# Optimization experiments

Hardware: AMD Instinct MI355X
Metric: run time of the kernel (lower is better)

The kernel has to match this reference:

```python
import jax, jax.numpy as jnp
import numpy as np

N = 100000   # nodes
E = 3200000  # edges
F = 128      # input features
H1 = 128     # first_gcn_dimensions
H2 = 64      # second_gcn_dimensions
D1 = 64      # first_dense_neurons
D2 = 8       # second_dense_neurons
L = 10       # number_of_labels


def setup_inputs() -> dict:
    key = jax.random.key(0)
    ks = jax.random.split(key, 8)
    edges = jax.random.randint(ks[0], (2, E), 0, N)
    features = jax.random.normal(ks[1], (N, F), dtype=jnp.float32)
    s = lambda k, shape: jax.random.normal(k, shape, dtype=jnp.float32) * 0.05
    return dict(
        edges=edges, features=features,
        W1=s(ks[2], (F, H1)), b1=jnp.zeros((H1,), jnp.float32),
        W2=s(ks[3], (H1, H2)), b2=jnp.zeros((H2,), jnp.float32),
        Wf1=s(ks[4], (H2, D1)), bf1=jnp.zeros((D1,), jnp.float32),
        Wf2=s(ks[5], (D1, D2)), bf2=jnp.zeros((D2,), jnp.float32),
        Wl=s(ks[6], (H2 * D2, L)), bl=jnp.zeros((L,), jnp.float32),
    )


def gcn_conv(x, W, b, src, dst, n):
    # PyG GCNConv: x' = D^{-1/2} (A + I) D^{-1/2} (x W) + b  (self-loops already in src/dst)
    h = x @ W                                            # [N, out]
    deg = jax.ops.segment_sum(jnp.ones(dst.shape[0], x.dtype), dst, num_segments=n)
    dinv = jnp.where(deg > 0, jax.lax.rsqrt(deg), 0.0)   # deg^{-1/2}, 0 for isolated
    norm = dinv[src] * dinv[dst]                         # [E+N]
    agg = jax.ops.segment_sum(h[src] * norm[:, None], dst, num_segments=n)
    return agg + b


def reference(edges, features, W1, b1, W2, b2, Wf1, bf1, Wf2, bf2, Wl, bl):
    n = features.shape[0]
    loop = jnp.arange(n)
    src = jnp.concatenate([edges[0], loop])
    dst = jnp.concatenate([edges[1], loop])

    h1 = jax.nn.relu(gcn_conv(features, W1, b1, src, dst, n))  # [N, H1]
    h2 = gcn_conv(h1, W2, b2, src, dst, n)                     # [N, H2]

    a1 = jnp.tanh(h2 @ Wf1 + bf1)                              # [N, D1]
    att = jax.nn.softmax(a1 @ Wf2 + bf2, axis=0)               # softmax over nodes, [N, D2]

    graph_embedding = (att.T @ h2).reshape(1, -1)              # [1, D2*H2]
    P = att.T @ att - jnp.eye(att.shape[1], dtype=att.dtype)   # [D2, D2]
    penalty = jnp.sum(jnp.sqrt(jnp.sum(P * P, axis=1)))

    predictions = jax.nn.log_softmax(graph_embedding @ Wl + bl, axis=1)  # [1, L]
    return graph_embedding, penalty, predictions
```

## Files before the change

kernel.cpp:

```cpp
#include <hip/hip_runtime.h>
#include <hip/hip_bf16.h>
#include <math.h>

#define NNODES 100000
#define NEDGES 3200000
#define NBUK ((NNODES + 127) >> 7)
#define NCHUNK 256
#define EPC (NEDGES / NCHUNK)

typedef float floatx2 __attribute__((ext_vector_type(2)));

__device__ __forceinline__ unsigned short f2bf(float x) {
    unsigned u = __float_as_uint(x);
    unsigned r = u + 0x7FFFu + ((u >> 16) & 1u);
    return (unsigned short)(r >> 16);
}
__device__ __forceinline__ void unpack8_bf16(uint4 v, float* f) {
    f[0] = __uint_as_float(v.x << 16); f[1] = __uint_as_float(v.x & 0xFFFF0000u);
    f[2] = __uint_as_float(v.y << 16); f[3] = __uint_as_float(v.y & 0xFFFF0000u);
    f[4] = __uint_as_float(v.z << 16); f[5] = __uint_as_float(v.z & 0xFFFF0000u);
    f[6] = __uint_as_float(v.w << 16); f[7] = __uint_as_float(v.w & 0xFFFF0000u);
}

__device__ __forceinline__ void acc8_fp8(uint2 v, floatx2* a) {
    a[0] += __builtin_amdgcn_cvt_pk_f32_fp8(v.x, false);
    a[1] += __builtin_amdgcn_cvt_pk_f32_fp8(v.x, true);
    a[2] += __builtin_amdgcn_cvt_pk_f32_fp8(v.y, false);
    a[3] += __builtin_amdgcn_cvt_pk_f32_fp8(v.y, true);
}
__device__ __forceinline__ void acc4_fp8(unsigned v, floatx2* a) {
    a[0] += __builtin_amdgcn_cvt_pk_f32_fp8(v, false);
    a[1] += __builtin_amdgcn_cvt_pk_f32_fp8(v, true);
}

__global__ __launch_bounds__(1024) void chunk_hist_kernel(const int* __restrict__ dst,
                                                          int* __restrict__ hist) {
    __shared__ int h[NBUK];
    int c = blockIdx.x, t = threadIdx.x;
    for (int i = t; i < NBUK; i += 1024) h[i] = 0;
    __syncthreads();
    int e0 = c * EPC, e1 = e0 + EPC;
    for (int e = e0 + t; e < e1; e += 1024)
        atomicAdd(&h[dst[e] >> 7], 1);
    __syncthreads();
    for (int i = t; i < NBUK; i += 1024)
        hist[c * NBUK + i] = h[i];
}

__global__ void col_scan_kernel(int* __restrict__ hist, int* __restrict__ btot) {
    int t = blockIdx.x * 256 + threadIdx.x;
    if (t >= NBUK) return;
    int run = 0;
    for (int c = 0; c < NCHUNK; c++) {
        int idx = c * NBUK + t;
        int v = hist[idx];
        hist[idx] = run;
        run += v;
    }
    btot[t] = run;
}

__global__ void bucket_scan_kernel(const int* __restrict__ btot, int* __restrict__ bstart,
                                   int* __restrict__ row_start, float* __restrict__ smalls) {
    __shared__ int s[1024];
    int t = threadIdx.x;
    if (t < 592) smalls[t] = 0.0f;
    int v = (t < NBUK) ? btot[t] : 0;
    s[t] = v;
    __syncthreads();
    for (int off = 1; off < 1024; off <<= 1) {
        int x = (t >= off) ? s[t - off] : 0;
        __syncthreads();
        s[t] += x;
        __syncthreads();
    }
    if (t < NBUK) bstart[t] = s[t] - v;
    if (t == 0) {
        bstart[NBUK] = NEDGES;
        row_start[NNODES] = NEDGES;
    }
}

__global__ __launch_bounds__(1024) void chunk_scatter_kernel(const int* __restrict__ src,
                                                             const int* __restrict__ dst,
                                                             const int* __restrict__ hist,
                                                             const int* __restrict__ bstart,
                                                             int* __restrict__ ebuk) {
    __shared__ int cur[NBUK];
    int c = blockIdx.x, t = threadIdx.x;
    for (int i = t; i < NBUK; i += 1024)
        cur[i] = bstart[i] + hist[c * NBUK + i];
    __syncthreads();
    int e0 = c * EPC, e1 = e0 + EPC;
    for (int e = e0 + t; e < e1; e += 1024) {
        int d = dst[e];
        int pos = atomicAdd(&cur[d >> 7], 1);
        ebuk[pos] = src[e] | ((d & 127) << 20);
    }
}

__global__ __launch_bounds__(256) void build_kernel(const int* __restrict__ ebuk,
                                                    const int* __restrict__ bstart,
                                                    int* __restrict__ row_start,
                                                    float* __restrict__ dinv,
                                                    int* __restrict__ csr) {
    __shared__ int cnt[128];
    __shared__ int scn[128];
    __shared__ int cur[128];
    int b = blockIdx.x;
    int t = threadIdx.x;
    int s0 = bstart[b], s1 = bstart[b + 1];
    if (t < 128) cnt[t] = 0;
    __syncthreads();
    for (int i = s0 + t; i < s1; i += 256)
        atomicAdd(&cnt[(ebuk[i] >> 20) & 127], 1);
    __syncthreads();
    if (t < 128) scn[t] = cnt[t];
    __syncthreads();
#pragma unroll
    for (int off = 1; off < 128; off <<= 1) {
        int x = (t < 128 && t >= off) ? scn[t - off] : 0;
        __syncthreads();
        if (t < 128) scn[t] += x;
        __syncthreads();
    }
    int node = b * 128 + t;
    if (t < 128) {
        int rs = s0 + scn[t] - cnt[t];
        cur[t] = rs;
        if (node < NNODES) {
            row_start[node] = rs;
            dinv[node] = rsqrtf((float)cnt[t] + 1.0f);
        }
    }
    __syncthreads();
    for (int i = s0 + t; i < s1; i += 256) {
        int v = ebuk[i];
        int pos = atomicAdd(&cur[(v >> 20) & 127], 1);
        csr[pos] = v & 0xFFFFF;
    }
}

template <int KIN, int KOUT, int TR>
__global__ __launch_bounds__(256) void gemm_stage_kernel(const float* __restrict__ A,
                                                         const float* __restrict__ W,
                                                         const float* __restrict__ rowscale,
                                                         unsigned char* __restrict__ stage,
                                                         int nrows) {
    constexpr int COLG = KOUT / 4;
    constexpr int ROWG = 256 / COLG;
    constexpr int R    = TR / ROWG;
    constexpr int LDK  = KIN + 4;
    __shared__ float As[TR][LDK];
    int block_row = blockIdx.x * TR;
    int tid = threadIdx.x;

    constexpr int C4 = KIN / 4;
    for (int idx = tid; idx < TR * C4; idx += 256) {
        int r = idx / C4, c = idx % C4;
        float4 v = make_float4(0.f, 0.f, 0.f, 0.f);
        if (block_row + r < nrows)
            v = *(const float4*)(A + (size_t)(block_row + r) * KIN + c * 4);
        *(float4*)(&As[r][c * 4]) = v;
    }
    __syncthreads();

    int cg = tid % COLG, rg = tid / COLG;
    int j  = cg * 4;
    int r0 = rg * R;
    float4 acc[R];
#pragma unroll
    for (int r = 0; r < R; r++) acc[r] = make_float4(0.f, 0.f, 0.f, 0.f);

#pragma unroll 4
    for (int k = 0; k < KIN; k++) {
        float4 w = *(const float4*)(W + (size_t)k * KOUT + j);
#pragma unroll
        for (int r = 0; r < R; r++) {
            float a = As[r0 + r][k];
            acc[r].x += a * w.x; acc[r].y += a * w.y;
            acc[r].z += a * w.z; acc[r].w += a * w.w;
        }
    }
#pragma unroll
    for (int r = 0; r < R; r++) {
        int row = block_row + r0 + r;
        if (row < nrows) {
            float d = rowscale[row];
            int pk = __builtin_amdgcn_cvt_pk_fp8_f32(acc[r].x * d, acc[r].y * d, 0, false);
            pk = __builtin_amdgcn_cvt_pk_fp8_f32(acc[r].z * d, acc[r].w * d, pk, true);
            *(unsigned*)(stage + (size_t)row * KOUT + j) = (unsigned)pk;
        }
    }
}

template <int KIN, int KOUT, int TR>
__global__ __launch_bounds__(256) void gemm_stage_bf16_kernel(const unsigned short* __restrict__ A,
                                                              const float* __restrict__ W,
                                                              const float* __restrict__ rowscale,
                                                              unsigned char* __restrict__ stage,
                                                              int nrows) {
    constexpr int COLG = KOUT / 4;
    constexpr int ROWG = 256 / COLG;
    constexpr int R    = TR / ROWG;
    constexpr int LDK  = KIN + 4;
    __shared__ float As[TR][LDK];
    int block_row = blockIdx.x * TR;
    int tid = threadIdx.x;

    constexpr int C8 = KIN / 8;
    for (int idx = tid; idx < TR * C8; idx += 256) {
        int r = idx / C8, c = idx % C8;
        float f[8];
        uint4 v = make_uint4(0, 0, 0, 0);
        if (block_row + r < nrows)
            v = *(const uint4*)(A + (size_t)(block_row + r) * KIN + c * 8);
        unpack8_bf16(v, f);
#pragma unroll
        for (int i = 0; i < 8; i++) As[r][c * 8 + i] = f[i];
    }
    __syncthreads();

    int cg = tid % COLG, rg = tid / COLG;
    int j  = cg * 4;
    int r0 = rg * R;
    float4 acc[R];
#pragma unroll
    for (int r = 0; r < R; r++) acc[r] = make_float4(0.f, 0.f, 0.f, 0.f);

#pragma unroll 4
    for (int k = 0; k < KIN; k++) {
        float4 w = *(const float4*)(W + (size_t)k * KOUT + j);
#pragma unroll
        for (int r = 0; r < R; r++) {
            float a = As[r0 + r][k];
            acc[r].x += a * w.x; acc[r].y += a * w.y;
            acc[r].z += a * w.z; acc[r].w += a * w.w;
        }
    }
#pragma unroll
    for (int r = 0; r < R; r++) {
        int row = block_row + r0 + r;
        if (row < nrows) {
            float d = rowscale[row];
            int pk = __builtin_amdgcn_cvt_pk_fp8_f32(acc[r].x * d, acc[r].y * d, 0, false);
            pk = __builtin_amdgcn_cvt_pk_fp8_f32(acc[r].z * d, acc[r].w * d, pk, true);
            *(unsigned*)(stage + (size_t)row * KOUT + j) = (unsigned)pk;
        }
    }
}

__global__ __launch_bounds__(256) void gather128_kernel(
    const unsigned char* __restrict__ hs, const int* __restrict__ row_start,
    const int* __restrict__ csr, const float* __restrict__ dinv,
    const float* __restrict__ bias, unsigned short* __restrict__ out) {
    int wave = threadIdx.x >> 6;
    int lane = threadIdx.x & 63;
    int n = blockIdx.x * 4 + wave;
    if (n >= NNODES) return;
    int g = lane >> 4;
    int c = lane & 15;
    unsigned boff = (unsigned)c << 3;
    int start = row_start[n], end = row_start[n + 1];
    floatx2 acc[4];
#pragma unroll
    for (int i = 0; i < 4; i++) acc[i] = (floatx2)(0.f);
    int w = (start + 3) & ~3;
    if (w > end) w = end;
    {
        int e2 = start + g;
        if (e2 < w) {
            unsigned o = ((unsigned)csr[e2] << 7) + boff;
            acc8_fp8(*(const uint2*)(hs + o), acc);
        }
    }
    for (; w + 32 <= end; w += 32) {
        int4 ca = *(const int4*)(csr + w + 4 * g);
        int4 cbv = *(const int4*)(csr + w + 16 + 4 * g);
        uint2 v0 = *(const uint2*)(hs + (((unsigned)ca.x  << 7) + boff));
        uint2 v1 = *(const uint2*)(hs + (((unsigned)ca.y  << 7) + boff));
        uint2 v2 = *(const uint2*)(hs + (((unsigned)ca.z  << 7) + boff));
        uint2 v3 = *(const uint2*)(hs + (((unsigned)ca.w  << 7) + boff));
        uint2 v4 = *(const uint2*)(hs + (((unsigned)cbv.x << 7) + boff));
        uint2 v5 = *(const uint2*)(hs + (((unsigned)cbv.y << 7) + boff));
        uint2 v6 = *(const uint2*)(hs + (((unsigned)cbv.z << 7) + boff));
        uint2 v7 = *(const uint2*)(hs + (((unsigned)cbv.w << 7) + boff));
        acc8_fp8(v0, acc); acc8_fp8(v1, acc); acc8_fp8(v2, acc); acc8_fp8(v3, acc);
        acc8_fp8(v4, acc); acc8_fp8(v5, acc); acc8_fp8(v6, acc); acc8_fp8(v7, acc);
    }
    for (; w + 16 <= end; w += 16) {
        int4 cs = *(const int4*)(csr + w + 4 * g);
        uint2 v0 = *(const uint2*)(hs + (((unsigned)cs.x << 7) + boff));
        uint2 v1 = *(const uint2*)(hs + (((unsigned)cs.y << 7) + boff));
        uint2 v2 = *(const uint2*)(hs + (((unsigned)cs.z << 7) + boff));
        uint2 v3 = *(const uint2*)(hs + (((unsigned)cs.w << 7) + boff));
        acc8_fp8(v0, acc); acc8_fp8(v1, acc); acc8_fp8(v2, acc); acc8_fp8(v3, acc);
    }
    for (int e2 = w + g; e2 < end; e2 += 4) {
        unsigned o = ((unsigned)csr[e2] << 7) + boff;
        acc8_fp8(*(const uint2*)(hs + o), acc);
    }
#pragma unroll
    for (int off = 16; off <= 32; off <<= 1)
#pragma unroll
        for (int i = 0; i < 4; i++) {
            acc[i].x += __shfl_xor(acc[i].x, off);
            acc[i].y += __shfl_xor(acc[i].y, off);
        }
    if (g == 0) {
        floatx2 s[4];
#pragma unroll
        for (int i = 0; i < 4; i++) s[i] = (floatx2)(0.f);
        acc8_fp8(*(const uint2*)(hs + (((unsigned)n << 7) + boff)), s);
        float d = dinv[n];
        int j = c * 8;
        float4 b0 = *(const float4*)(bias + j);
        float4 b1 = *(const float4*)(bias + j + 4);
        float r0 = fmaxf((acc[0].x + s[0].x) * d + b0.x, 0.f);
        float r1 = fmaxf((acc[0].y + s[0].y) * d + b0.y, 0.f);
        float r2 = fmaxf((acc[1].x + s[1].x) * d + b0.z, 0.f);
        float r3 = fmaxf((acc[1].y + s[1].y) * d + b0.w, 0.f);
        float r4 = fmaxf((acc[2].x + s[2].x) * d + b1.x, 0.f);
        float r5 = fmaxf((acc[2].y + s[2].y) * d + b1.y, 0.f);
        float r6 = fmaxf((acc[3].x + s[3].x) * d + b1.z, 0.f);
        float r7 = fmaxf((acc[3].y + s[3].y) * d + b1.w, 0.f);
        uint4 p;
        p.x = (unsigned)f2bf(r0) | ((unsigned)f2bf(r1) << 16);
        p.y = (unsigned)f2bf(r2) | ((unsigned)f2bf(r3) << 16);
        p.z = (unsigned)f2bf(r4) | ((unsigned)f2bf(r5) << 16);
        p.w = (unsigned)f2bf(r6) | ((unsigned)f2bf(r7) << 16);
        *(uint4*)(out + (((size_t)n << 7) + j)) = p;
    }
}

__global__ __launch_bounds__(256) void gather64_kernel(
    const unsigned char* __restrict__ hs, const int* __restrict__ row_start,
    const int* __restrict__ csr, const float* __restrict__ dinv,
    const float* __restrict__ bias, float* __restrict__ out) {
    int wave = threadIdx.x >> 6;
    int lane = threadIdx.x & 63;
    int n = blockIdx.x * 4 + wave;
    if (n >= NNODES) return;
    int g = lane >> 4;
    int c = lane & 15;
    unsigned boff = (unsigned)c << 2;
    int start = row_start[n], end = row_start[n + 1];
    floatx2 acc[2];
    acc[0] = (floatx2)(0.f); acc[1] = (floatx2)(0.f);
    int w = (start + 3) & ~3;
    if (w > end) w = end;
    {
        int e2 = start + g;
        if (e2 < w) {
            unsigned o = ((unsigned)csr[e2] << 6) + boff;
            acc4_fp8(*(const unsigned*)(hs + o), acc);
        }
    }
    for (; w + 32 <= end; w += 32) {
        int4 ca = *(const int4*)(csr + w + 4 * g);
        int4 cbv = *(const int4*)(csr + w + 16 + 4 * g);
        unsigned v0 = *(const unsigned*)(hs + (((unsigned)ca.x  << 6) + boff));
        unsigned v1 = *(const unsigned*)(hs + (((unsigned)ca.y  << 6) + boff));
        unsigned v2 = *(const unsigned*)(hs + (((unsigned)ca.z  << 6) + boff));
        unsigned v3 = *(const unsigned*)(hs + (((unsigned)ca.w  << 6) + boff));
        unsigned v4 = *(const unsigned*)(hs + (((unsigned)cbv.x << 6) + boff));
        unsigned v5 = *(const unsigned*)(hs + (((unsigned)cbv.y << 6) + boff));
        unsigned v6 = *(const unsigned*)(hs + (((unsigned)cbv.z << 6) + boff));
        unsigned v7 = *(const unsigned*)(hs + (((unsigned)cbv.w << 6) + boff));
        acc4_fp8(v0, acc); acc4_fp8(v1, acc); acc4_fp8(v2, acc); acc4_fp8(v3, acc);
        acc4_fp8(v4, acc); acc4_fp8(v5, acc); acc4_fp8(v6, acc); acc4_fp8(v7, acc);
    }
    for (; w + 16 <= end; w += 16) {
        int4 cs = *(const int4*)(csr + w + 4 * g);
        unsigned v0 = *(const unsigned*)(hs + (((unsigned)cs.x << 6) + boff));
        unsigned v1 = *(const unsigned*)(hs + (((unsigned)cs.y << 6) + boff));
        unsigned v2 = *(const unsigned*)(hs + (((unsigned)cs.z << 6) + boff));
        unsigned v3 = *(const unsigned*)(hs + (((unsigned)cs.w << 6) + boff));
        acc4_fp8(v0, acc); acc4_fp8(v1, acc); acc4_fp8(v2, acc); acc4_fp8(v3, acc);
    }
    for (int e2 = w + g; e2 < end; e2 += 4) {
        unsigned o = ((unsigned)csr[e2] << 6) + boff;
        acc4_fp8(*(const unsigned*)(hs + o), acc);
    }
#pragma unroll
    for (int off = 16; off <= 32; off <<= 1)
#pragma unroll
        for (int i = 0; i < 2; i++) {
            acc[i].x += __shfl_xor(acc[i].x, off);
            acc[i].y += __shfl_xor(acc[i].y, off);
        }
    if (g == 0) {
        floatx2 s[2];
        s[0] = (floatx2)(0.f); s[1] = (floatx2)(0.f);
        acc4_fp8(*(const unsigned*)(hs + (((unsigned)n << 6) + boff)), s);
        float d = dinv[n];
        int j = c * 4;
        float4 b4 = *(const float4*)(bias + j);
        float4 r;
        r.x = (acc[0].x + s[0].x) * d + b4.x;
        r.y = (acc[0].y + s[0].y) * d + b4.y;
        r.z = (acc[1].x + s[1].x) * d + b4.z;
        r.w = (acc[1].y + s[1].y) * d + b4.w;
        *(float4*)(out + (((size_t)n << 6) + j)) = r;
    }
}

__global__ __launch_bounds__(256) void attnpool_kernel(const float* __restrict__ h2,
                                                       const float* __restrict__ Wf1,
                                                       const float* __restrict__ bf1,
                                                       const float* __restrict__ Wf2,
                                                       const float* __restrict__ bf2,
                                                       float* __restrict__ ge,
                                                       float* __restrict__ ata,
                                                       float* __restrict__ colsum) {
    __shared__ float h2S[64][68];
    __shared__ float a1S[64][68];
    __shared__ float attS[64][8];
    __shared__ float colS[8][64];
    int t = threadIdx.x;
    int d0 = t >> 6;
    int j  = t & 63;
    int de = t >> 3, ee = t & 7;
    float accge0 = 0.f, accge1 = 0.f, accata = 0.f, acccol = 0.f;
    int ntiles = (NNODES + 63) / 64;
    for (int tile = blockIdx.x; tile < ntiles; tile += gridDim.x) {
        int base = tile * 64;
#pragma unroll
        for (int q = 0; q < 4; q++) {
            int idx = t + q * 256;
            int r = idx >> 4, cc = (idx & 15) * 4;
            int row = base + r;
            float4 v = (row < NNODES) ? *(const float4*)(h2 + (size_t)row * 64 + cc)
                                      : make_float4(0.f, 0.f, 0.f, 0.f);
            *(float4*)(&h2S[r][cc]) = v;
        }
        __syncthreads();
        {
            int cg = t & 15, rg = t >> 4;
            int jj = cg * 4, r0 = rg * 4;
            float4 b4 = *(const float4*)(bf1 + jj);
            float4 acc[4];
#pragma unroll
            for (int r = 0; r < 4; r++) acc[r] = b4;
#pragma unroll 4
            for (int k = 0; k < 64; k++) {
                float4 wv = *(const float4*)(Wf1 + (size_t)k * 64 + jj);
#pragma unroll
                for (int r = 0; r < 4; r++) {
                    float a = h2S[r0 + r][k];
                    acc[r].x += a * wv.x; acc[r].y += a * wv.y;
                    acc[r].z += a * wv.z; acc[r].w += a * wv.w;
                }
            }
#pragma unroll
            for (int r = 0; r < 4; r++) {
                a1S[r0 + r][jj]     = tanhf(acc[r].x);
                a1S[r0 + r][jj + 1] = tanhf(acc[r].y);
                a1S[r0 + r][jj + 2] = tanhf(acc[r].z);
                a1S[r0 + r][jj + 3] = tanhf(acc[r].w);
            }
        }
        __syncthreads();
        {
            int cc = t & 7, r = t >> 3;
#pragma unroll
            for (int h = 0; h < 2; h++) {
                int rr = r + h * 32;
                float acc = bf2[cc];
                for (int k = 0; k < 64; k++)
                    acc += a1S[rr][k] * Wf2[(size_t)k * 8 + cc];
                float ev = (base + rr < NNODES) ? __expf(acc) : 0.f;
                attS[rr][cc] = ev;
                colS[cc][rr] = ev;
            }
        }
        __syncthreads();
#pragma unroll 8
        for (int i = 0; i < 64; i++) {
            float hv = h2S[i][j];
            accge0 += attS[i][d0] * hv;
            accge1 += attS[i][d0 + 4] * hv;
        }
        if (t < 64) {
#pragma unroll 8
            for (int i = 0; i < 64; i++) accata += attS[i][de] * attS[i][ee];
        }
        if (t < 8) {
            float s = 0.f;
#pragma unroll
            for (int r = 0; r < 64; r++) s += colS[t][r];
            acccol += s;
        }
        __syncthreads();
    }
    atomicAdd(ge + d0 * 64 + j, accge0);
    atomicAdd(ge + (d0 + 4) * 64 + j, accge1);
    if (t < 64) atomicAdd(ata + de * 8 + ee, accata);
    if (t < 8) atomicAdd(colsum + t, acccol);
}

__global__ void final_kernel(const float* __restrict__ geacc, const float* __restrict__ ata,
                             const float* __restrict__ colsum, const float* __restrict__ Wl,
                             const float* __restrict__ bl, float* __restrict__ out) {
    __shared__ float geF[512];
    __shared__ float inv[8];
    __shared__ float logits[10];
    int t = threadIdx.x;
    if (t < 8) inv[t] = 1.0f / colsum[t];
    __syncthreads();
    for (int idx = t; idx < 512; idx += 64) {
        int d = idx >> 6;
        float v = geacc[idx] * inv[d];
        geF[idx] = v;
        out[idx] = v;
    }
    __syncthreads();
    if (t == 0) {
        float pen = 0.f;
        for (int d = 0; d < 8; d++) {
            float s = 0.f;
            for (int e = 0; e < 8; e++) {
                float p = ata[d * 8 + e] * inv[d] * inv[e] - (d == e ? 1.0f : 0.0f);
                s += p * p;
            }
            pen += sqrtf(s);
        }
        out[512] = pen;
    }
    if (t < 10) {
        float acc = bl[t];
        for (int k = 0; k < 512; k++) acc += geF[k] * Wl[(size_t)k * 10 + t];
        logits[t] = acc;
    }
    __syncthreads();
    if (t == 0) {
        float m = -INFINITY;
        for (int l = 0; l < 10; l++) m = fmaxf(m, logits[l]);
        float s = 0.f;
        for (int l = 0; l < 10; l++) s += expf(logits[l] - m);
        float ls = logf(s);
        for (int l = 0; l < 10; l++) out[513 + l] = logits[l] - m - ls;
    }
}

extern "C" void kernel_launch(void* const* d_in, const int* in_sizes, int n_in,
                              void* d_out, int out_size, void* d_ws, size_t ws_size,
                              hipStream_t stream) {
    const int* esrc = (const int*)d_in[0];
    const int* edst = esrc + NEDGES;
    const float* X   = (const float*)d_in[1];
    const float* W1  = (const float*)d_in[2];
    const float* b1  = (const float*)d_in[3];
    const float* W2  = (const float*)d_in[4];
    const float* b2  = (const float*)d_in[5];
    const float* Wf1 = (const float*)d_in[6];
    const float* bf1 = (const float*)d_in[7];
    const float* Wf2 = (const float*)d_in[8];
    const float* bf2 = (const float*)d_in[9];
    const float* Wl  = (const float*)d_in[10];
    const float* bl  = (const float*)d_in[11];
    float* out = (float*)d_out;

    float* ws     = (float*)d_ws;
    float* dinv   = ws;
    float* smalls = ws + 100352;
    float* colsum = smalls + 8;
    float* ata    = smalls + 16;
    float* geacc  = smalls + 80;
    float* A = ws + 101376;
    float* B = A + (size_t)NNODES * 128;
    int* row_start = (int*)(B + (size_t)NNODES * 128);
    int* btot      = row_start + 100352;
    int* bstart    = btot + 1024;
    int* csr       = bstart + 1024;
    int* ebuk      = (int*)A;
    int* hist      = (int*)B;
    unsigned char* stage = (unsigned char*)A;
    unsigned short* h1 = (unsigned short*)B;
    float* h2  = B;

    chunk_hist_kernel<<<NCHUNK, 1024, 0, stream>>>(edst, hist);
    col_scan_kernel<<<4, 256, 0, stream>>>(hist, btot);
    bucket_scan_kernel<<<1, 1024, 0, stream>>>(btot, bstart, row_start, smalls);
    chunk_scatter_kernel<<<NCHUNK, 1024, 0, stream>>>(esrc, edst, hist, bstart, ebuk);
    build_kernel<<<NBUK, 256, 0, stream>>>(ebuk, bstart, row_start, dinv, csr);

    gemm_stage_kernel<128, 128, 64><<<(NNODES + 63) / 64, 256, 0, stream>>>(X, W1, dinv, stage, NNODES);
    gather128_kernel<<<(NNODES + 3) / 4, 256, 0, stream>>>(stage, row_start, csr, dinv, b1, h1);

    gemm_stage_bf16_kernel<128, 64, 64><<<(NNODES + 63) / 64, 256, 0, stream>>>(h1, W2, dinv, stage, NNODES);
    gather64_kernel<<<(NNODES + 3) / 4, 256, 0, stream>>>(stage, row_start, csr, dinv, b2, h2);

    attnpool_kernel<<<512, 256, 0, stream>>>(h2, Wf1, bf1, Wf2, bf2, geacc, ata, colsum);
    final_kernel<<<1, 64, 0, stream>>>(geacc, ata, colsum, Wl, bl, out);
}
```

Before: 489.5 us.

## Use bf16 MFMA for both GCN GEMMs and vectorize edge histogram/scatter loads

Replaces the scalar FP32 FMA GEMM kernels with a bf16 MFMA (16x16x32) kernel. It stages transposed bf16 weights, prepared by a new prep kernel, and bf16 A tiles in LDS, then writes results through an LDS C tile before fp8 packing. The edge histogram and scatter kernels now read src/dst as int4 vectors. The aim is to move the dense transforms onto matrix cores and cut load instruction count in preprocessing. In exchange, the first GEMM's input features are rounded to bf16, which reduces precision.

```diff
diff --git a/kernel.cpp b/kernel.cpp
--- a/kernel.cpp
+++ b/kernel.cpp
@@ -9,17 +9,13 @@
 #define EPC (NEDGES / NCHUNK)
 
 typedef float floatx2 __attribute__((ext_vector_type(2)));
+typedef float f32x4 __attribute__((ext_vector_type(4)));
+typedef short bf16x8 __attribute__((ext_vector_type(8)));
 
 __device__ __forceinline__ unsigned short f2bf(float x) {
     unsigned u = __float_as_uint(x);
     unsigned r = u + 0x7FFFu + ((u >> 16) & 1u);
     return (unsigned short)(r >> 16);
-}
-__device__ __forceinline__ void unpack8_bf16(uint4 v, float* f) {
-    f[0] = __uint_as_float(v.x << 16); f[1] = __uint_as_float(v.x & 0xFFFF0000u);
-    f[2] = __uint_as_float(v.y << 16); f[3] = __uint_as_float(v.y & 0xFFFF0000u);
-    f[4] = __uint_as_float(v.z << 16); f[5] = __uint_as_float(v.z & 0xFFFF0000u);
-    f[6] = __uint_as_float(v.w << 16); f[7] = __uint_as_float(v.w & 0xFFFF0000u);
 }
 
 __device__ __forceinline__ void acc8_fp8(uint2 v, floatx2* a) {
@@ -33,15 +29,33 @@
     a[1] += __builtin_amdgcn_cvt_pk_f32_fp8(v, true);
 }
 
+__global__ void prep_w_kernel(const float* __restrict__ W1, const float* __restrict__ W2,
+                              unsigned short* __restrict__ Wt1, unsigned short* __restrict__ Wt2) {
+    int i = blockIdx.x * 256 + threadIdx.x;
+    if (i < 128 * 128) {
+        int k = i >> 7, n = i & 127;
+        Wt1[n * 128 + k] = f2bf(W1[i]);
+    } else if (i < 128 * 128 + 128 * 64) {
+        int j = i - 128 * 128;
+        int k = j >> 6, n = j & 63;
+        Wt2[n * 128 + k] = f2bf(W2[j]);
+    }
+}
+
 __global__ __launch_bounds__(1024) void chunk_hist_kernel(const int* __restrict__ dst,
                                                           int* __restrict__ hist) {
     __shared__ int h[NBUK];
     int c = blockIdx.x, t = threadIdx.x;
     for (int i = t; i < NBUK; i += 1024) h[i] = 0;
     __syncthreads();
-    int e0 = c * EPC, e1 = e0 + EPC;
-    for (int e = e0 + t; e < e1; e += 1024)
-        atomicAdd(&h[dst[e] >> 7], 1);
+    const int4* d4 = (const int4*)(dst + c * EPC);
+    for (int i = t; i < EPC / 4; i += 1024) {
+        int4 d = d4[i];
+        atomicAdd(&h[d.x >> 7], 1);
+        atomicAdd(&h[d.y >> 7], 1);
+        atomicAdd(&h[d.z >> 7], 1);
+        atomicAdd(&h[d.w >> 7], 1);
+    }
     __syncthreads();
     for (int i = t; i < NBUK; i += 1024)
         hist[c * NBUK + i] = h[i];
@@ -91,11 +105,19 @@
     for (int i = t; i < NBUK; i += 1024)
         cur[i] = bstart[i] + hist[c * NBUK + i];
     __syncthreads();
-    int e0 = c * EPC, e1 = e0 + EPC;
-    for (int e = e0 + t; e < e1; e += 1024) {
-        int d = dst[e];
-        int pos = atomicAdd(&cur[d >> 7], 1);
-        ebuk[pos] = src[e] | ((d & 127) << 20);
+    const int4* s4 = (const int4*)(src + c * EPC);
+    const int4* d4 = (const int4*)(dst + c * EPC);
+    for (int i = t; i < EPC / 4; i += 1024) {
+        int4 s = s4[i];
+        int4 d = d4[i];
+        int p0 = atomicAdd(&cur[d.x >> 7], 1);
+        ebuk[p0] = s.x | ((d.x & 127) << 20);
+        int p1 = atomicAdd(&cur[d.y >> 7], 1);
+        ebuk[p1] = s.y | ((d.y & 127) << 20);
+        int p2 = atomicAdd(&cur[d.z >> 7], 1);
+        ebuk[p2] = s.z | ((d.z & 127) << 20);
+        int p3 = atomicAdd(&cur[d.w >> 7], 1);
+        ebuk[p3] = s.w | ((d.w & 127) << 20);
     }
 }
 
@@ -141,111 +163,86 @@
     }
 }
 
-template <int KIN, int KOUT, int TR>
-__global__ __launch_bounds__(256) void gemm_stage_kernel(const float* __restrict__ A,
-                                                         const float* __restrict__ W,
-                                                         const float* __restrict__ rowscale,
-                                                         unsigned char* __restrict__ stage,
-                                                         int nrows) {
-    constexpr int COLG = KOUT / 4;
-    constexpr int ROWG = 256 / COLG;
-    constexpr int R    = TR / ROWG;
-    constexpr int LDK  = KIN + 4;
-    __shared__ float As[TR][LDK];
-    int block_row = blockIdx.x * TR;
-    int tid = threadIdx.x;
-
-    constexpr int C4 = KIN / 4;
-    for (int idx = tid; idx < TR * C4; idx += 256) {
-        int r = idx / C4, c = idx % C4;
-        float4 v = make_float4(0.f, 0.f, 0.f, 0.f);
-        if (block_row + r < nrows)
-            v = *(const float4*)(A + (size_t)(block_row + r) * KIN + c * 4);
-        *(float4*)(&As[r][c * 4]) = v;
-    }
-    __syncthreads();
-
-    int cg = tid % COLG, rg = tid / COLG;
-    int j  = cg * 4;
-    int r0 = rg * R;
-    float4 acc[R];
-#pragma unroll
-    for (int r = 0; r < R; r++) acc[r] = make_float4(0.f, 0.f, 0.f, 0.f);
-
-#pragma unroll 4
-    for (int k = 0; k < KIN; k++) {
-        float4 w = *(const float4*)(W + (size_t)k * KOUT + j);
-#pragma unroll
-        for (int r = 0; r < R; r++) {
-            float a = As[r0 + r][k];
-            acc[r].x += a * w.x; acc[r].y += a * w.y;
-            acc[r].z += a * w.z; acc[r].w += a * w.w;
-        }
-    }
-#pragma unroll
-    for (int r = 0; r < R; r++) {
-        int row = block_row + r0 + r;
-        if (row < nrows) {
+template <int KIN, int KOUT, bool ABF16>
+__global__ __launch_bounds__(256) void gemm_mfma_kernel(const void* __restrict__ Av,
+                                                        const unsigned short* __restrict__ Wt,
+                                                        const float* __restrict__ rowscale,
+                                                        unsigned char* __restrict__ stage) {
+    constexpr int LDK = KIN + 8;
+    constexpr int LDC = KOUT + 4;
+    constexpr int SH_AB = (64 + KOUT) * LDK * 2;
+    constexpr int SH_C  = 64 * LDC * 4;
+    constexpr int SH = SH_AB > SH_C ? SH_AB : SH_C;
+    __shared__ char shbuf[SH];
+    unsigned short* As = (unsigned short*)shbuf;
+    unsigned short* Ws = As + 64 * LDK;
+    float* Cs = (float*)shbuf;
+    int t = threadIdx.x;
+    int block_row = blockIdx.x * 64;
+
+    for (int idx = t; idx < KOUT * (KIN / 8); idx += 256) {
+        int n = idx / (KIN / 8), c = idx % (KIN / 8);
+        *(uint4*)(Ws + n * LDK + c * 8) = *(const uint4*)(Wt + n * KIN + c * 8);
+    }
+    if (ABF16) {
+        const unsigned short* A = (const unsigned short*)Av;
+        for (int idx = t; idx < 64 * (KIN / 8); idx += 256) {
+            int r = idx / (KIN / 8), c = idx % (KIN / 8);
+            uint4 v = make_uint4(0, 0, 0, 0);
+            if (block_row + r < NNODES)
+                v = *(const uint4*)(A + (size_t)(block_row + r) * KIN + c * 8);
+            *(uint4*)(As + r * LDK + c * 8) = v;
+        }
+    } else {
+        const float* A = (const float*)Av;
+        for (int idx = t; idx < 64 * (KIN / 4); idx += 256) {
+            int r = idx / (KIN / 4), c = idx % (KIN / 4);
+            float4 v = make_float4(0.f, 0.f, 0.f, 0.f);
+            if (block_row + r < NNODES)
+                v = *(const float4*)(A + (size_t)(block_row + r) * KIN + c * 4);
+            unsigned p0 = (unsigned)f2bf(v.x) | ((unsigned)f2bf(v.y) << 16);
+            unsigned p1 = (unsigned)f2bf(v.z) | ((unsigned)f2bf(v.w) << 16);
+            *(uint2*)(As + r * LDK + c * 4) = make_uint2(p0, p1);
+        }
+    }
+    __syncthreads();
+
+    int wv = t >> 6, lane = t & 63;
+    int r0 = wv * 16;
+    int m = lane & 15, q = lane >> 4;
+    constexpr int NT = KOUT / 16;
+    constexpr int KS = KIN / 32;
+    f32x4 acc[NT];
+#pragma unroll
+    for (int nt = 0; nt < NT; nt++) acc[nt] = (f32x4)(0.f);
+    bf16x8 afr[KS];
+#pragma unroll
+    for (int ks = 0; ks < KS; ks++)
+        afr[ks] = *(bf16x8*)(As + (r0 + m) * LDK + ks * 32 + q * 8);
+#pragma unroll
+    for (int nt = 0; nt < NT; nt++) {
+#pragma unroll
+        for (int ks = 0; ks < KS; ks++) {
+            bf16x8 b = *(bf16x8*)(Ws + (nt * 16 + m) * LDK + ks * 32 + q * 8);
+            acc[nt] = __builtin_amdgcn_mfma_f32_16x16x32_bf16(afr[ks], b, acc[nt], 0, 0, 0);
+        }
+    }
+    __syncthreads();
+#pragma unroll
+    for (int nt = 0; nt < NT; nt++)
+#pragma unroll
+        for (int j = 0; j < 4; j++)
+            Cs[(r0 + q * 4 + j) * LDC + nt * 16 + m] = acc[nt][j];
+    __syncthreads();
+    for (int idx = t; idx < 64 * (KOUT / 4); idx += 256) {
+        int r = idx / (KOUT / 4), c4 = idx % (KOUT / 4);
+        int row = block_row + r;
+        if (row < NNODES) {
+            float4 v = *(float4*)(Cs + r * LDC + c4 * 4);
             float d = rowscale[row];
-            int pk = __builtin_amdgcn_cvt_pk_fp8_f32(acc[r].x * d, acc[r].y * d, 0, false);
-            pk = __builtin_amdgcn_cvt_pk_fp8_f32(acc[r].z * d, acc[r].w * d, pk, true);
-            *(unsigned*)(stage + (size_t)row * KOUT + j) = (unsigned)pk;
-        }
-    }
-}
-
-template <int KIN, int KOUT, int TR>
-__global__ __launch_bounds__(256) void gemm_stage_bf16_kernel(const unsigned short* __restrict__ A,
-                                                              const float* __restrict__ W,
-                                                              const float* __restrict__ rowscale,
-                                                              unsigned char* __restrict__ stage,
-                                                              int nrows) {
-    constexpr int COLG = KOUT / 4;
-    constexpr int ROWG = 256 / COLG;
-    constexpr int R    = TR / ROWG;
-    constexpr int LDK  = KIN + 4;
-    __shared__ float As[TR][LDK];
-    int block_row = blockIdx.x * TR;
-    int tid = threadIdx.x;
-
-    constexpr int C8 = KIN / 8;
-    for (int idx = tid; idx < TR * C8; idx += 256) {
-        int r = idx / C8, c = idx % C8;
-        float f[8];
-        uint4 v = make_uint4(0, 0, 0, 0);
-        if (block_row + r < nrows)
-            v = *(const uint4*)(A + (size_t)(block_row + r) * KIN + c * 8);
-        unpack8_bf16(v, f);
-#pragma unroll
-        for (int i = 0; i < 8; i++) As[r][c * 8 + i] = f[i];
-    }
-    __syncthreads();
-
-    int cg = tid % COLG, rg = tid / COLG;
-    int j  = cg * 4;
-    int r0 = rg * R;
-    float4 acc[R];
-#pragma unroll
-    for (int r = 0; r < R; r++) acc[r] = make_float4(0.f, 0.f, 0.f, 0.f);
-
-#pragma unroll 4
-    for (int k = 0; k < KIN; k++) {
-        float4 w = *(const float4*)(W + (size_t)k * KOUT + j);
-#pragma unroll
-        for (int r = 0; r < R; r++) {
-            float a = As[r0 + r][k];
-            acc[r].x += a * w.x; acc[r].y += a * w.y;
-            acc[r].z += a * w.z; acc[r].w += a * w.w;
-        }
-    }
-#pragma unroll
-    for (int r = 0; r < R; r++) {
-        int row = block_row + r0 + r;
-        if (row < nrows) {
-            float d = rowscale[row];
-            int pk = __builtin_amdgcn_cvt_pk_fp8_f32(acc[r].x * d, acc[r].y * d, 0, false);
-            pk = __builtin_amdgcn_cvt_pk_fp8_f32(acc[r].z * d, acc[r].w * d, pk, true);
-            *(unsigned*)(stage + (size_t)row * KOUT + j) = (unsigned)pk;
+            int pk = __builtin_amdgcn_cvt_pk_fp8_f32(v.x * d, v.y * d, 0, false);
+            pk = __builtin_amdgcn_cvt_pk_fp8_f32(v.z * d, v.w * d, pk, true);
+            *(unsigned*)(stage + (size_t)row * KOUT + c4 * 4) = (unsigned)pk;
         }
     }
 }
@@ -573,22 +570,26 @@
     int* btot      = row_start + 100352;
     int* bstart    = btot + 1024;
     int* csr       = bstart + 1024;
+    unsigned short* Wt1 = (unsigned short*)(csr + NEDGES);
+    unsigned short* Wt2 = Wt1 + 128 * 128;
     int* ebuk      = (int*)A;
     int* hist      = (int*)B;
     unsigned char* stage = (unsigned char*)A;
     unsigned short* h1 = (unsigned short*)B;
     float* h2  = B;
 
+    prep_w_kernel<<<96, 256, 0, stream>>>(W1, W2, Wt1, Wt2);
+
     chunk_hist_kernel<<<NCHUNK, 1024, 0, stream>>>(edst, hist);
     col_scan_kernel<<<4, 256, 0, stream>>>(hist, btot);
     bucket_scan_kernel<<<1, 1024, 0, stream>>>(btot, bstart, row_start, smalls);
     chunk_scatter_kernel<<<NCHUNK, 1024, 0, stream>>>(esrc, edst, hist, bstart, ebuk);
     build_kernel<<<NBUK, 256, 0, stream>>>(ebuk, bstart, row_start, dinv, csr);
 
-    gemm_stage_kernel<128, 128, 64><<<(NNODES + 63) / 64, 256, 0, stream>>>(X, W1, dinv, stage, NNODES);
+    gemm_mfma_kernel<128, 128, false><<<(NNODES + 63) / 64, 256, 0, stream>>>(X, Wt1, dinv, stage);
     gather128_kernel<<<(NNODES + 3) / 4, 256, 0, stream>>>(stage, row_start, csr, dinv, b1, h1);
 
-    gemm_stage_bf16_kernel<128, 64, 64><<<(NNODES + 63) / 64, 256, 0, stream>>>(h1, W2, dinv, stage, NNODES);
+    gemm_mfma_kernel<128, 64, true><<<(NNODES + 63) / 64, 256, 0, stream>>>(h1, Wt2, dinv, stage);
     gather64_kernel<<<(NNODES + 3) / 4, 256, 0, stream>>>(stage, row_start, csr, dinv, b2, h2);
 
     attnpool_kernel<<<512, 256, 0, stream>>>(h2, Wf1, bf1, Wf2, bf2, geacc, ata, colsum);
```

Measured after the change: 430.9 us. 12.0% less time.
